# Optimization experiments

Hardware: AMD Instinct MI355X
Metric: run time of the kernel (lower is better)

Reference implementation:

```python
import jax, jax.numpy as jnp
import numpy as np


def _ln(z, g, b, eps=1e-5):
    mu = z.mean(-1, keepdims=True)
    v = ((z - mu) ** 2).mean(-1, keepdims=True)
    return (z - mu) / jnp.sqrt(v + eps) * g + b


def _forward(x, C_prev, n_prev, m_prev, ln_in_g, ln_in_b, wq, bq, wk, bk, wv, bv, wi, bi, wf, bf, wo, bo, rd_w1, rd_b1, rd_g, rd_be, rd_w2, rd_b2, ssm_log_lam, ssm_log_b, ssm_c, ssm_log_d, ssm_log_step, ssm_vol_gate, ssm_alpha, ssm_ln_g, ssm_ln_b, ln_mem_g, ln_mem_b):
    B, S, F = x.shape
    D = wq.shape[0]
    sqd = jnp.sqrt(jnp.float32(D))
    w = max(1, int(S * 0.2))
    pad0 = jnp.zeros((B, 1, F), x.dtype)
    cs = jnp.concatenate([pad0, jnp.cumsum(x, 1)], 1)
    cs2 = jnp.concatenate([pad0, jnp.cumsum(x * x, 1)], 1)
    wsum = cs[:, w:] - cs[:, :-w]
    wsq = cs2[:, w:] - cs2[:, :-w]
    var = (wsq - wsum * wsum / w) / (w - 1)
    std = jnp.sqrt(jnp.clip(var, 0.0))
    vol = jnp.concatenate([jnp.broadcast_to(std[:, :1], (B, w - 1, F)), std], 1)
    sv = vol.mean(2, keepdims=True)
    sv = sv / (sv.mean(1, keepdims=True) + 1e-6)  # [B,S,1]
    # --- parallel gate computation ---
    xn = _ln(x, ln_in_g, ln_in_b)
    regime = jax.nn.softmax(jax.nn.gelu(_ln(xn @ rd_w1.T + rd_b1, rd_g, rd_be), approximate=False) @ rd_w2.T + rd_b2, axis=-1)
    q = xn @ wq.T + bq
    k = (xn @ wk.T + bk) / sqd
    v = xn @ wv.T + bv
    it = xn @ wi.T + bi  # [B,S,1]
    ft = xn @ wf.T + bf
    o = jax.nn.sigmoid(xn @ wo.T + bo)
    # --- stabilize_gates (running-max exponential stabilization) ---
    mp = jnp.clip(m_prev, -100.0, 100.0)[:, None, :]  # [B,1,1]
    m_t = jnp.maximum(ft, mp + ft)
    ig = jnp.exp(jnp.clip(it - m_t, -15.0, 15.0))
    fg = jnp.exp(jnp.clip(ft + mp - m_t, -15.0, 15.0))
    # --- store_key_value outer products + cumulative matrix memory ---
    kn = k / (jnp.linalg.norm(k, axis=2, keepdims=True) + 1e-12) * sqd
    vn = v / (jnp.linalg.norm(v, axis=2, keepdims=True) + 1e-6) * sqd
    upd = jnp.clip(ig, 0.0, 1.0)[..., None] * (vn[..., :, None] * kn[..., None, :])  # [B,S,D,D]
    f_cum = jnp.cumprod(fg, axis=1)  # [B,S,1]
    C_t = f_cum[..., None] * C_prev[:, None] + jnp.cumsum(upd, 1)
    # --- structured state-space mixing, vectorized over the D memory rows ---
    lam = -jnp.exp(ssm_log_lam)
    step = jnp.exp(ssm_log_step)
    a_disc = (2.0 + step * lam) / (2.0 - step * lam)  # bilinear discretization
    b_disc = step * (1.0 + a_disc) * jnp.exp(ssm_log_b)[:, 0] / 2.0
    xr = C_t.transpose(0, 2, 1, 3).reshape(B * D, S, D)  # rows folded into batch
    volr = jnp.broadcast_to(sv[:, None, :, 0], (B, D, S)).reshape(B * D, S)
    u = xr.mean(-1)  # [BD,S], per-step scalar drive
    vgate = jax.nn.sigmoid(ssm_vol_gate)
    def stepf(h, inp):
        u_t, vol_t = inp
        h = a_disc[None] * h + b_disc[None] * u_t[:, None]
        h = _ln(h, ssm_ln_g, ssm_ln_b)
        h = h / (1.0 + vgate[None] * vol_t[:, None])
        return h, h
    h0 = jnp.zeros((B * D, D), x.dtype)
    _, hs = jax.lax.scan(stepf, h0, (u.T, volr.T))  # [S,BD,D]
    yscal = jnp.einsum('sbn,n->bs', hs, ssm_c[0])  # [BD,S]
    y = yscal[..., None] + jnp.exp(ssm_log_d) * xr
    alpha = jax.nn.sigmoid(ssm_alpha)
    mixed = alpha * xr + (1.0 - alpha) * y
    C_mixed = mixed.reshape(B, D, S, D).transpose(0, 2, 1, 3)
    mf = regime[:, :, 0:1][..., None]  # regime-aware mixing factor
    C_t = C_mixed * mf + C_t * (1.0 - mf)
    C_t = C_t / (jnp.linalg.norm(C_t.reshape(B, S, D * D), axis=-1)[..., None, None] + 1e-6) * sqd
    # --- mLSTM readout (stabilizer_threshold = 1.0) ---
    n_t = f_cum * n_prev[:, None, :] + jnp.cumsum(ig * k, 1)
    h_til = jnp.einsum('bsij,bsj->bsi', C_t, q)
    denom = jnp.maximum(jnp.abs(jnp.sum(n_t * q, -1, keepdims=True)), 1.0)
    return o * _ln(h_til / denom, ln_mem_g, ln_mem_b)


def setup_inputs() -> dict:
    key = jax.random.key(0)
    ks = jax.random.split(key, 12)
    B, S, F, D = 8, 512, 32, 64
    sF, sD = 1.0 / np.sqrt(F), 1.0 / np.sqrt(D)
    n = lambda k, sh, s=1.0: jax.random.normal(k, sh, jnp.float32) * s
    return dict(
        x=n(ks[0], (B, S, F)),
        C_prev=jnp.zeros((B, D, D), jnp.float32),
        n_prev=jnp.zeros((B, D), jnp.float32),
        m_prev=jnp.zeros((B, 1), jnp.float32),
        ln_in_g=jnp.ones((F,), jnp.float32), ln_in_b=jnp.zeros((F,), jnp.float32),
        wq=n(ks[1], (D, F), sF), bq=jnp.zeros((D,), jnp.float32),
        wk=n(ks[2], (D, F), sF), bk=jnp.zeros((D,), jnp.float32),
        wv=n(ks[3], (D, F), sF), bv=jnp.zeros((D,), jnp.float32),
        wi=n(ks[4], (1, F), sF), bi=jnp.zeros((1,), jnp.float32),
        wf=n(ks[5], (1, F), sF), bf=jnp.ones((1,), jnp.float32),
        wo=n(ks[6], (D, F), sF), bo=jnp.zeros((D,), jnp.float32),
        rd_w1=n(ks[7], (D, F), sF), rd_b1=jnp.zeros((D,), jnp.float32),
        rd_g=jnp.ones((D,), jnp.float32), rd_be=jnp.zeros((D,), jnp.float32),
        rd_w2=n(ks[8], (4, D), sD), rd_b2=jnp.zeros((4,), jnp.float32),
        ssm_log_lam=jnp.linspace(np.log(0.001), np.log(0.1), D).astype(jnp.float32),
        ssm_log_b=jax.random.uniform(ks[9], (D, 1), jnp.float32, -0.5, 0.5),
        ssm_c=n(ks[10], (1, D), sD),
        ssm_log_d=jnp.zeros((1,), jnp.float32),
        ssm_log_step=jnp.float32(np.log(0.001)),
        ssm_vol_gate=jnp.ones((D,), jnp.float32),
        ssm_alpha=jnp.float32(0.7),
        ssm_ln_g=jnp.ones((D,), jnp.float32), ssm_ln_b=jnp.zeros((D,), jnp.float32),
        ln_mem_g=jnp.ones((D,), jnp.float32), ln_mem_b=jnp.zeros((D,), jnp.float32),
    )


def reference(x, C_prev, n_prev, m_prev, ln_in_g, ln_in_b, wq, bq, wk, bk, wv, bv, wi, bi, wf, bf, wo, bo, rd_w1, rd_b1, rd_g, rd_be, rd_w2, rd_b2, ssm_log_lam, ssm_log_b, ssm_c, ssm_log_d, ssm_log_step, ssm_vol_gate, ssm_alpha, ssm_ln_g, ssm_ln_b, ln_mem_g, ln_mem_b):
    return _forward(x, C_prev, n_prev, m_prev, ln_in_g, ln_in_b, wq, bq, wk, bk, wv, bv, wi, bi, wf, bf, wo, bo, rd_w1, rd_b1, rd_g, rd_be, rd_w2, rd_b2, ssm_log_lam, ssm_log_b, ssm_c, ssm_log_d, ssm_log_step, ssm_vol_gate, ssm_alpha, ssm_ln_g, ssm_ln_b, ln_mem_g, ln_mem_b)
```

## Files before the change

kernel.cpp:

```cpp
#include <hip/hip_runtime.h>
#include <math.h>

#define BB 8
#define SS 512
#define FF 32
#define DD 64
#define WVOL 102
#define CH 16
#define NCH (SS / CH)

template<int CTRL, int RM, bool BC>
__device__ __forceinline__ float updpp(float oldv, float x) {
  return __int_as_float(__builtin_amdgcn_update_dpp(
      __float_as_int(oldv), __float_as_int(x), CTRL, RM, 0xF, BC));
}
__device__ __forceinline__ float rlane(float v, int l) {
  return __int_as_float(__builtin_amdgcn_readlane(__float_as_int(v), l));
}
__device__ __forceinline__ float dsum64(float x) {
  x += updpp<0x111, 0xF, true>(0.f, x);
  x += updpp<0x112, 0xF, true>(0.f, x);
  x += updpp<0x114, 0xF, true>(0.f, x);
  x += updpp<0x118, 0xF, true>(0.f, x);
  x += updpp<0x142, 0xF, true>(0.f, x);
  x += updpp<0x143, 0xF, true>(0.f, x);
  return rlane(x, 63);
}
__device__ __forceinline__ float dsum32(float x) {
  x += updpp<0x111, 0xF, true>(0.f, x);
  x += updpp<0x112, 0xF, true>(0.f, x);
  x += updpp<0x114, 0xF, true>(0.f, x);
  x += updpp<0x118, 0xF, true>(0.f, x);
  x += updpp<0x142, 0xF, true>(0.f, x);
  return rlane(x, 31);
}
__device__ __forceinline__ float dscan_add(float x) {
  x += updpp<0x111, 0xF, true>(0.f, x);
  x += updpp<0x112, 0xF, true>(0.f, x);
  x += updpp<0x114, 0xF, true>(0.f, x);
  x += updpp<0x118, 0xF, true>(0.f, x);
  x += updpp<0x142, 0xA, true>(0.f, x);
  x += updpp<0x143, 0xC, true>(0.f, x);
  return x;
}
__device__ __forceinline__ float dscan_mul(float x) {
  x *= updpp<0x111, 0xF, false>(1.f, x);
  x *= updpp<0x112, 0xF, false>(1.f, x);
  x *= updpp<0x114, 0xF, false>(1.f, x);
  x *= updpp<0x118, 0xF, false>(1.f, x);
  x *= updpp<0x142, 0xA, false>(1.f, x);
  x *= updpp<0x143, 0xC, false>(1.f, x);
  return x;
}

__global__ void k_vol_std(const float* __restrict__ x, float* __restrict__ svraw) {
  int b = blockIdx.x; int s = WVOL - 1 + blockIdx.y;
  int lane = threadIdx.x; int f = lane & 31; int half = lane >> 5;
  const float* xb = x + (size_t)(b * SS) * FF + f;
  float wsum = 0.f, wsq = 0.f;
  int t0 = s - WVOL + 1 + half;
#pragma unroll 17
  for (int k = 0; k < WVOL / 2; ++k) {
    float xv = xb[(t0 + 2 * k) * FF];
    wsum += xv; wsq = fmaf(xv, xv, wsq);
  }
  wsum += __shfl_xor(wsum, 32); wsq += __shfl_xor(wsq, 32);
  float var = (wsq - wsum * wsum * (1.f / WVOL)) * (1.f / (WVOL - 1));
  float sd = sqrtf(fmaxf(var, 0.f));
  float m = dsum64(sd) * 0.5f * (1.f / FF);
  if (lane == 0) svraw[b * SS + s] = m;
}

__global__ void k_proj(const float* __restrict__ x, const float* __restrict__ m_prev,
                       const float* __restrict__ Cp,
                       const float* __restrict__ ln_in_g, const float* __restrict__ ln_in_b,
                       const float* __restrict__ wq, const float* __restrict__ bq,
                       const float* __restrict__ wk, const float* __restrict__ bk,
                       const float* __restrict__ wv, const float* __restrict__ bv,
                       const float* __restrict__ wi, const float* __restrict__ bi,
                       const float* __restrict__ wf, const float* __restrict__ bf,
                       const float* __restrict__ wo, const float* __restrict__ bo,
                       const float* __restrict__ rd_w1, const float* __restrict__ rd_b1,
                       const float* __restrict__ rd_g, const float* __restrict__ rd_be,
                       const float* __restrict__ rd_w2, const float* __restrict__ rd_b2,
                       float* __restrict__ qo, float* __restrict__ kno, float* __restrict__ vno,
                       float* __restrict__ iko, float* __restrict__ oo,
                       float* __restrict__ knT, float* __restrict__ vnT,
                       float* __restrict__ cg_a, float* __restrict__ fg_a,
                       float* __restrict__ mf_a, float* __restrict__ cks_a,
                       float* __restrict__ qsum_a, float* __restrict__ zc) {
  int bs = blockIdx.x; int b = bs / SS; int s = bs % SS;
  int lane = threadIdx.x;
  __shared__ float xs[FF];
  __shared__ float ks[DD];
  float xv = (lane < FF) ? x[bs * FF + lane] : 0.f;
  float s1x = dsum32(xv);
  float s2x = dsum32(xv * xv);
  if (lane < FF) {
    float mu = s1x * (1.f / FF);
    float var = s2x * (1.f / FF) - mu * mu;
    xs[lane] = (xv - mu) * rsqrtf(var + 1e-5f) * ln_in_g[lane] + ln_in_b[lane];
  }
  __syncthreads();
  int d = lane;
  float aq = bq[d], ak = bk[d], av = bv[d], ao = bo[d], at = rd_b1[d];
#pragma unroll
  for (int f = 0; f < FF; ++f) {
    float xf = xs[f];
    aq = fmaf(xf, wq[d * FF + f], aq);
    ak = fmaf(xf, wk[d * FF + f], ak);
    av = fmaf(xf, wv[d * FF + f], av);
    ao = fmaf(xf, wo[d * FF + f], ao);
    at = fmaf(xf, rd_w1[d * FF + f], at);
  }
  float pit = (lane < FF) ? xs[lane] * wi[lane] : 0.f;
  float pft = (lane < FF) ? xs[lane] * wf[lane] : 0.f;
  float itv = dsum32(pit) + bi[0];
  float ftv = dsum32(pft) + bf[0];
  float s1 = dsum64(at), s2 = dsum64(at * at);
  float mu = s1 * (1.f / DD);
  float var = s2 * (1.f / DD) - mu * mu;
  float tn = (at - mu) * rsqrtf(var + 1e-5f) * rd_g[d] + rd_be[d];
  float ge = 0.5f * tn * (1.f + erff(tn * 0.70710678118654752f));
  float l0 = dsum64(ge * rd_w2[0 * DD + d]) + rd_b2[0];
  float l1 = dsum64(ge * rd_w2[1 * DD + d]) + rd_b2[1];
  float l2 = dsum64(ge * rd_w2[2 * DD + d]) + rd_b2[2];
  float l3 = dsum64(ge * rd_w2[3 * DD + d]) + rd_b2[3];
  float mx = fmaxf(fmaxf(l0, l1), fmaxf(l2, l3));
  float e0 = expf(l0 - mx), e1 = expf(l1 - mx), e2 = expf(l2 - mx), e3 = expf(l3 - mx);
  float mfv = e0 / (e0 + e1 + e2 + e3);
  float kd = ak * 0.125f;
  float kk = dsum64(kd * kd);
  float knd = kd * (8.f / (sqrtf(kk) + 1e-12f));
  float vv = dsum64(av * av);
  float vnd = av * (8.f / (sqrtf(vv) + 1e-6f));
  float ksum = dsum64(knd);
  float qsum = dsum64(aq);
  float mp = fminf(fmaxf(m_prev[b], -100.f), 100.f);
  float mt = fmaxf(ftv, mp + ftv);
  float ig = expf(fminf(fmaxf(itv - mt, -15.f), 15.f));
  float fg = expf(fminf(fmaxf(ftv + mp - mt, -15.f), 15.f));
  float cg = fminf(ig, 1.f);
  qo[bs * DD + d] = aq;
  kno[bs * DD + d] = knd;
  vno[bs * DD + d] = vnd;
  iko[bs * DD + d] = ig * kd;
  oo[bs * DD + d] = 1.f / (1.f + expf(-ao));
  knT[(b * DD + d) * SS + s] = knd;
  vnT[(b * DD + d) * SS + s] = vnd;
  ks[d] = knd;
  __syncthreads();
  float acc = 0.f;
  const float* cr = Cp + (b * DD + d) * DD;
#pragma unroll
  for (int j = 0; j < DD; ++j) acc = fmaf(cr[j], ks[j], acc);
  float z = dsum64(vnd * acc);
  if (lane == 0) {
    cg_a[bs] = cg; fg_a[bs] = fg; mf_a[bs] = mfv;
    cks_a[bs] = cg * ksum; qsum_a[bs] = qsum;
    zc[bs] = cg * z;
  }
}

__global__ void k_main(const float* __restrict__ qo, const float* __restrict__ kno,
                       const float* __restrict__ vno,
                       const float* __restrict__ knT, const float* __restrict__ vnT,
                       const float* __restrict__ cg_a,
                       float* __restrict__ p2, float* __restrict__ rho) {
  int bs = blockIdx.x; int b = bs / SS; int s = bs % SS;
  int lane = threadIdx.x;
  __shared__ float w[64];
  const float* qrow = qo + bs * DD;
  const float* krow = kno + bs * DD;
  const float* vrow = vno + bs * DD;
  float pacc = 0.f, rp = 0.f;
  int sT = s & ~63;
  for (int T = 0; T < sT; T += 64) {
    int t = T + lane;
    float A = 0.f, KK = 0.f, VV = 0.f;
#pragma unroll 8
    for (int j = 0; j < DD; ++j) {
      float kt = knT[(b * DD + j) * SS + t];
      float vt = vnT[(b * DD + j) * SS + t];
      A = fmaf(kt, qrow[j], A);
      KK = fmaf(kt, krow[j], KK);
      VV = fmaf(vt, vrow[j], VV);
    }
    float cgt = cg_a[b * SS + t];
    w[lane] = cgt * A;
    rp = fmaf(2.f * cgt, KK * VV, rp);
    __syncthreads();
#pragma unroll 8
    for (int tl = 0; tl < 64; ++tl)
      pacc = fmaf(w[tl], vno[(b * SS + T + tl) * DD + lane], pacc);
    __syncthreads();
  }
  {
    int T = sT; int t = T + lane;
    float A = 0.f, KK = 0.f, VV = 0.f;
#pragma unroll 8
    for (int j = 0; j < DD; ++j) {
      float kt = knT[(b * DD + j) * SS + t];
      float vt = vnT[(b * DD + j) * SS + t];
      A = fmaf(kt, qrow[j], A);
      KK = fmaf(kt, krow[j], KK);
      VV = fmaf(vt, vrow[j], VV);
    }
    float cgt = cg_a[b * SS + t];
    w[lane] = (t <= s) ? cgt * A : 0.f;
    float wr = (t < s) ? 2.f : (t == s ? 1.f : 0.f);
    rp = fmaf(wr * cgt, KK * VV, rp);
    __syncthreads();
    int tmax = s - sT;
    for (int tl = 0; tl <= tmax; ++tl)
      pacc = fmaf(w[tl], vno[(b * SS + T + tl) * DD + lane], pacc);
  }
  p2[bs * DD + lane] = pacc;
  float rr = dsum64(rp);
  if (lane == 0) rho[bs] = cg_a[bs] * rr;
}

__global__ void k_scalar_scan(const float* __restrict__ fg_a, const float* __restrict__ zc,
                              const float* __restrict__ rho, const float* __restrict__ Cp,
                              const float* __restrict__ svraw,
                              float* __restrict__ fcum, float* __restrict__ cpd,
                              float* __restrict__ sn2, float* __restrict__ cpr,
                              float* __restrict__ cpn2, float* __restrict__ sv) {
  int b = blockIdx.x; int lane = threadIdx.x;
  float rs = 0.f, r2 = 0.f;
  const float* cr = Cp + (b * DD + lane) * DD;
#pragma unroll
  for (int j = 0; j < DD; ++j) { float c = cr[j]; rs += c; r2 = fmaf(c, c, r2); }
  cpr[b * DD + lane] = rs;
  float tot2 = dsum64(r2);
  if (lane == 0) cpn2[b] = tot2;
  float m0 = svraw[b * SS + WVOL - 1];
  float vals[8]; float part = 0.f;
#pragma unroll
  for (int c = 0; c < 8; ++c) {
    int idx = c * 64 + lane;
    float v = (idx < WVOL - 1) ? m0 : svraw[b * SS + idx];
    vals[c] = v; part += v;
  }
  float tot = dsum64(part);
  float inv = 1.f / (tot * (1.f / SS) + 1e-6f);
#pragma unroll
  for (int c = 0; c < 8; ++c) sv[b * SS + c * 64 + lane] = vals[c] * inv;
  float cf = 1.f, cz = 0.f, crr = 0.f;
  for (int c = 0; c < 8; ++c) {
    int bs = b * SS + c * 64 + lane;
    float f = dscan_mul(fg_a[bs]) * cf;
    float z = dscan_add(zc[bs]) + cz;
    float r = dscan_add(rho[bs]) + crr;
    fcum[bs] = f; cpd[bs] = z; sn2[bs] = r;
    cf = rlane(f, 63); cz = rlane(z, 63); crr = rlane(r, 63);
  }
}

__global__ void k_csum(const float* __restrict__ ik, const float* __restrict__ vno,
                       const float* __restrict__ cks_a,
                       float* __restrict__ csn, float* __restrict__ csr) {
  int blk = blockIdx.x; int b = blk / NCH; int w = blk % NCH; int d = threadIdx.x;
  float na = 0.f, ra = 0.f;
#pragma unroll
  for (int t = 0; t < CH; ++t) {
    int bs = b * SS + w * CH + t;
    na += ik[bs * DD + d];
    ra = fmaf(cks_a[bs], vno[bs * DD + d], ra);
  }
  csn[blk * DD + d] = na; csr[blk * DD + d] = ra;
}
__global__ void k_scan_apply(const float* __restrict__ ik, const float* __restrict__ vno,
                             const float* __restrict__ cks_a,
                             const float* __restrict__ csn, const float* __restrict__ csr,
                             float* __restrict__ nacc, float* __restrict__ racc) {
  int blk = blockIdx.x; int b = blk / NCH; int w = blk % NCH; int d = threadIdx.x;
  float na = 0.f, ra = 0.f;
  for (int w2 = 0; w2 < w; ++w2) {
    na += csn[(b * NCH + w2) * DD + d];
    ra += csr[(b * NCH + w2) * DD + d];
  }
#pragma unroll
  for (int t = 0; t < CH; ++t) {
    int bs = b * SS + w * CH + t;
    na += ik[bs * DD + d];
    ra = fmaf(cks_a[bs], vno[bs * DD + d], ra);
    nacc[bs * DD + d] = na;
    racc[bs * DD + d] = ra;
  }
}

__global__ void k_ssm(const float* __restrict__ fcum, const float* __restrict__ racc,
                      const float* __restrict__ cpr, const float* __restrict__ sv,
                      const float* __restrict__ log_lam, const float* __restrict__ log_b,
                      const float* __restrict__ cvec,
                      const float* __restrict__ log_step, const float* __restrict__ vol_gate,
                      const float* __restrict__ ln_g, const float* __restrict__ ln_b,
                      float* __restrict__ ysT) {
  int blk = blockIdx.x; int b = blk >> 6; int i = blk & 63;
  int n = threadIdx.x;
  float st = expf(log_step[0]);
  float lam = -expf(log_lam[n]);
  float ad = (2.f + st * lam) / (2.f - st * lam);
  float bd = st * (1.f + ad) * expf(log_b[n]) * 0.5f;
  float vg = 1.f / (1.f + expf(-vol_gate[n]));
  float g = ln_g[n], be = ln_b[n], cn = cvec[n];
  float cprv = cpr[b * DD + i];
  float u[8], w[8];
#pragma unroll
  for (int c = 0; c < 8; ++c) {
    int s = c * 64 + n; int bs = b * SS + s;
    u[c] = fmaf(fcum[bs], cprv, racc[(size_t)bs * DD + i]) * (1.f / DD);
    w[c] = sv[bs];
  }
  float h = 0.f;
#pragma unroll
  for (int c = 0; c < 8; ++c) {
    float yout = 0.f;
#pragma unroll 4
    for (int t = 0; t < 64; ++t) {
      float uu = rlane(u[c], t);
      float vv = rlane(w[c], t);
      float bdu = bd * uu;
      float rden = __builtin_amdgcn_rcpf(fmaf(vg, vv, 1.f));
      float grden = g * rden, berden = be * rden;
      float ht = fmaf(ad, h, bdu);
      float p1 = ht, p2 = ht * ht;
      p1 += updpp<0x111, 0xF, true>(0.f, p1); p2 += updpp<0x111, 0xF, true>(0.f, p2);
      p1 += updpp<0x112, 0xF, true>(0.f, p1); p2 += updpp<0x112, 0xF, true>(0.f, p2);
      p1 += updpp<0x114, 0xF, true>(0.f, p1); p2 += updpp<0x114, 0xF, true>(0.f, p2);
      p1 += updpp<0x118, 0xF, true>(0.f, p1); p2 += updpp<0x118, 0xF, true>(0.f, p2);
      p1 += updpp<0x142, 0xF, true>(0.f, p1); p2 += updpp<0x142, 0xF, true>(0.f, p2);
      p1 += updpp<0x143, 0xF, true>(0.f, p1); p2 += updpp<0x143, 0xF, true>(0.f, p2);
      float s1 = rlane(p1, 63), s2 = rlane(p2, 63);
      float mu = s1 * (1.f / DD);
      float r2m = fmaf(-mu, s1, s2);
      float arg = fmaxf(fmaf(r2m, 1.f / DD, 1e-5f), 1e-5f);
      float irs = __builtin_amdgcn_rsqf(arg);
      float hv = fmaf((ht - mu) * grden, irs, berden);
      h = hv;
      float y = cn * hv;
      y += updpp<0x111, 0xF, true>(0.f, y);
      y += updpp<0x112, 0xF, true>(0.f, y);
      y += updpp<0x114, 0xF, true>(0.f, y);
      y += updpp<0x118, 0xF, true>(0.f, y);
      y += updpp<0x142, 0xF, true>(0.f, y);
      y += updpp<0x143, 0xF, true>(0.f, y);
      float su = rlane(y, 63);
      yout = (n == t) ? su : yout;
    }
    ysT[(size_t)(b * DD + i) * SS + c * 64 + n] = yout;
  }
}

__global__ void k_final(const float* __restrict__ qo, const float* __restrict__ oo,
                        const float* __restrict__ p2, const float* __restrict__ racc,
                        const float* __restrict__ nacc, const float* __restrict__ ysT,
                        const float* __restrict__ Cp, const float* __restrict__ cpr,
                        const float* __restrict__ cpn2,
                        const float* __restrict__ fcum, const float* __restrict__ cpd,
                        const float* __restrict__ sn2,
                        const float* __restrict__ mf_a, const float* __restrict__ qsum_a,
                        const float* __restrict__ n_prev,
                        const float* __restrict__ ssm_log_d, const float* __restrict__ ssm_alpha,
                        const float* __restrict__ ln_mem_g, const float* __restrict__ ln_mem_b,
                        float* __restrict__ out) {
  int bs = blockIdx.x; int b = bs / SS; int s = bs % SS;
  int i = threadIdx.x;
  __shared__ float qv[DD];
  float qi = qo[bs * DD + i];
  qv[i] = qi;
  __syncthreads();
  float P1 = 0.f;
  const float* cr = Cp + (b * DD + i) * DD;
#pragma unroll
  for (int j = 0; j < DD; ++j) P1 = fmaf(cr[j], qv[j], P1);
  float fc = fcum[bs];
  float p = fmaf(fc, P1, p2[bs * DD + i]);
  float r = fmaf(fc, cpr[b * DD + i], racc[bs * DD + i]);
  float R2 = fc * fc * cpn2[b] + 2.f * fc * cpd[bs] + sn2[bs];
  float al = 1.f / (1.f + expf(-ssm_alpha[0]));
  float kap = al + (1.f - al) * expf(ssm_log_d[0]);
  float mfv = mf_a[bs];
  float beta = 1.f + mfv * (kap - 1.f);
  float gam = mfv * (1.f - al);
  float y = ysT[(size_t)(b * DD + i) * SS + s];
  float syr = dsum64(y * r);
  float sy2 = dsum64(y * y);
  float nrm2 = fmaxf(beta * beta * R2 + 2.f * beta * gam * syr + gam * gam * (float)DD * sy2, 0.f);
  float scale = 8.f / (sqrtf(nrm2) + 1e-6f);
  float nt = fmaf(fc, n_prev[b * DD + i], nacc[bs * DD + i]);
  float ndp = dsum64(nt * qi);
  float denom = fmaxf(fabsf(ndp), 1.f);
  float hh = scale * (fmaf(beta, p, gam * y * qsum_a[bs])) / denom;
  float s1 = dsum64(hh), s2 = dsum64(hh * hh);
  float mu = s1 * (1.f / DD);
  float var = fmaxf(s2 * (1.f / DD) - mu * mu, 0.f);
  float o = (hh - mu) * rsqrtf(var + 1e-5f) * ln_mem_g[i] + ln_mem_b[i];
  out[bs * DD + i] = oo[bs * DD + i] * o;
}

extern "C" void kernel_launch(void* const* d_in, const int* in_sizes, int n_in,
                              void* d_out, int out_size, void* d_ws, size_t ws_size,
                              hipStream_t stream) {
  const float* x        = (const float*)d_in[0];
  const float* C_prev   = (const float*)d_in[1];
  const float* n_prev   = (const float*)d_in[2];
  const float* m_prev   = (const float*)d_in[3];
  const float* ln_in_g  = (const float*)d_in[4];
  const float* ln_in_b  = (const float*)d_in[5];
  const float* wq = (const float*)d_in[6];  const float* bq = (const float*)d_in[7];
  const float* wk = (const float*)d_in[8];  const float* bk = (const float*)d_in[9];
  const float* wv = (const float*)d_in[10]; const float* bv = (const float*)d_in[11];
  const float* wi = (const float*)d_in[12]; const float* bi = (const float*)d_in[13];
  const float* wf = (const float*)d_in[14]; const float* bf = (const float*)d_in[15];
  const float* wo = (const float*)d_in[16]; const float* bo = (const float*)d_in[17];
  const float* rd_w1 = (const float*)d_in[18]; const float* rd_b1 = (const float*)d_in[19];
  const float* rd_g  = (const float*)d_in[20]; const float* rd_be = (const float*)d_in[21];
  const float* rd_w2 = (const float*)d_in[22]; const float* rd_b2 = (const float*)d_in[23];
  const float* ssm_log_lam  = (const float*)d_in[24];
  const float* ssm_log_b    = (const float*)d_in[25];
  const float* ssm_c        = (const float*)d_in[26];
  const float* ssm_log_d    = (const float*)d_in[27];
  const float* ssm_log_step = (const float*)d_in[28];
  const float* ssm_vol_gate = (const float*)d_in[29];
  const float* ssm_alpha    = (const float*)d_in[30];
  const float* ssm_ln_g     = (const float*)d_in[31];
  const float* ssm_ln_b     = (const float*)d_in[32];
  const float* ln_mem_g     = (const float*)d_in[33];
  const float* ln_mem_b     = (const float*)d_in[34];
  float* out = (float*)d_out;

  float* W = (float*)d_ws;
  size_t o0 = 0;
  const size_t BS = (size_t)BB * SS, BSD = BS * DD;
  float* sv    = W + o0; o0 += BS;
  float* svraw = W + o0; o0 += BS;
  float* qo   = W + o0; o0 += BSD;
  float* kno  = W + o0; o0 += BSD;
  float* vno  = W + o0; o0 += BSD;
  float* iko  = W + o0; o0 += BSD;
  float* oo   = W + o0; o0 += BSD;
  float* knT  = W + o0; o0 += BSD;
  float* vnT  = W + o0; o0 += BSD;
  float* p2   = W + o0; o0 += BSD;
  float* racc = W + o0; o0 += BSD;
  float* nacc = W + o0; o0 += BSD;
  float* ysT  = W + o0; o0 += BSD;
  float* cg_a = W + o0; o0 += BS;
  float* fg_a = W + o0; o0 += BS;
  float* mf_a = W + o0; o0 += BS;
  float* cks  = W + o0; o0 += BS;
  float* qsum = W + o0; o0 += BS;
  float* zc   = W + o0; o0 += BS;
  float* fcum = W + o0; o0 += BS;
  float* cpd  = W + o0; o0 += BS;
  float* rho  = W + o0; o0 += BS;
  float* sn2  = W + o0; o0 += BS;
  float* cpr  = W + o0; o0 += (size_t)BB * DD;
  float* cpn2 = W + o0; o0 += BB;
  float* csn  = W + o0; o0 += (size_t)BB * NCH * DD;
  float* csr  = W + o0; o0 += (size_t)BB * NCH * DD;

  hipLaunchKernelGGL(k_vol_std, dim3(BB, SS - WVOL + 1), dim3(64), 0, stream, x, svraw);
  hipLaunchKernelGGL(k_proj, dim3(BB * SS), dim3(64), 0, stream,
                     x, m_prev, C_prev, ln_in_g, ln_in_b, wq, bq, wk, bk, wv, bv, wi, bi,
                     wf, bf, wo, bo, rd_w1, rd_b1, rd_g, rd_be, rd_w2, rd_b2,
                     qo, kno, vno, iko, oo, knT, vnT, cg_a, fg_a, mf_a, cks, qsum, zc);
  hipLaunchKernelGGL(k_main, dim3(BB * SS), dim3(64), 0, stream,
                     qo, kno, vno, knT, vnT, cg_a, p2, rho);
  hipLaunchKernelGGL(k_scalar_scan, dim3(BB), dim3(64), 0, stream,
                     fg_a, zc, rho, C_prev, svraw, fcum, cpd, sn2, cpr, cpn2, sv);
  hipLaunchKernelGGL(k_csum, dim3(BB * NCH), dim3(64), 0, stream,
                     iko, vno, cks, csn, csr);
  hipLaunchKernelGGL(k_scan_apply, dim3(BB * NCH), dim3(64), 0, stream,
                     iko, vno, cks, csn, csr, nacc, racc);
  hipLaunchKernelGGL(k_ssm, dim3(BB * DD), dim3(64), 0, stream,
                     fcum, racc, cpr, sv, ssm_log_lam, ssm_log_b, ssm_c,
                     ssm_log_step, ssm_vol_gate, ssm_ln_g, ssm_ln_b, ysT);
  hipLaunchKernelGGL(k_final, dim3(BB * SS), dim3(64), 0, stream,
                     qo, oo, p2, racc, nacc, ysT, C_prev, cpr, cpn2, fcum, cpd, sn2,
                     mf_a, qsum, n_prev, ssm_log_d, ssm_alpha, ln_mem_g, ln_mem_b, out);
}
```

Before: 332.3 us.

## Tile causal attention-like main kernel over query rows and transpose weights for coalescing

The main causal kernel now handles 4 query rows per block and stages the V tile in shared memory, so each K/V column load is reused across rows. Blocks are interleaved short/long to balance the triangular workload. A new prep kernel transposes C_prev and the projection weights so per-lane reads in k_proj and k_final are coalesced. It also moves the C_prev row sums into the prep kernel and merges the scalar scan with the chunk-sum kernel to cut launches. In exchange the main kernel launches 4x fewer blocks, which may lower occupancy.

```diff
diff --git a/kernel.cpp b/kernel.cpp
--- a/kernel.cpp
+++ b/kernel.cpp
@@ -8,6 +8,7 @@
 #define WVOL 102
 #define CH 16
 #define NCH (SS / CH)
+#define QR 4
 
 template<int CTRL, int RM, bool BC>
 __device__ __forceinline__ float updpp(float oldv, float x) {
@@ -51,6 +52,42 @@
   x *= updpp<0x142, 0xA, false>(1.f, x);
   x *= updpp<0x143, 0xC, false>(1.f, x);
   return x;
+}
+
+__global__ void k_prep(const float* __restrict__ Cp,
+                       const float* __restrict__ wq, const float* __restrict__ wk,
+                       const float* __restrict__ wv, const float* __restrict__ wo,
+                       const float* __restrict__ rw1,
+                       float* __restrict__ CpT, float* __restrict__ wqT,
+                       float* __restrict__ wkT, float* __restrict__ wvT,
+                       float* __restrict__ woT, float* __restrict__ rw1T,
+                       float* __restrict__ cpr, float* __restrict__ cpn2) {
+  int blk = blockIdx.x; int lane = threadIdx.x;
+  if (blk < BB) {
+    int b = blk;
+    const float* rowp = Cp + (size_t)(b * DD + lane) * DD;
+    float rs = 0.f, r2 = 0.f;
+#pragma unroll 8
+    for (int j = 0; j < DD; ++j) {
+      float c = rowp[j];
+      rs += c; r2 = fmaf(c, c, r2);
+      CpT[(size_t)(b * DD + j) * DD + lane] = c;
+    }
+    cpr[b * DD + lane] = rs;
+    float tot2 = dsum64(r2);
+    if (lane == 0) cpn2[b] = tot2;
+  } else {
+    const float* src; float* dst;
+    switch (blk - BB) {
+      case 0: src = wq;  dst = wqT;  break;
+      case 1: src = wk;  dst = wkT;  break;
+      case 2: src = wv;  dst = wvT;  break;
+      case 3: src = wo;  dst = woT;  break;
+      default: src = rw1; dst = rw1T; break;
+    }
+#pragma unroll 8
+    for (int f = 0; f < FF; ++f) dst[f * DD + lane] = src[lane * FF + f];
+  }
 }
 
 __global__ void k_vol_std(const float* __restrict__ x, float* __restrict__ svraw) {
@@ -72,15 +109,15 @@
 }
 
 __global__ void k_proj(const float* __restrict__ x, const float* __restrict__ m_prev,
-                       const float* __restrict__ Cp,
+                       const float* __restrict__ CpT,
                        const float* __restrict__ ln_in_g, const float* __restrict__ ln_in_b,
-                       const float* __restrict__ wq, const float* __restrict__ bq,
-                       const float* __restrict__ wk, const float* __restrict__ bk,
-                       const float* __restrict__ wv, const float* __restrict__ bv,
+                       const float* __restrict__ wqT, const float* __restrict__ bq,
+                       const float* __restrict__ wkT, const float* __restrict__ bk,
+                       const float* __restrict__ wvT, const float* __restrict__ bv,
                        const float* __restrict__ wi, const float* __restrict__ bi,
                        const float* __restrict__ wf, const float* __restrict__ bf,
-                       const float* __restrict__ wo, const float* __restrict__ bo,
-                       const float* __restrict__ rd_w1, const float* __restrict__ rd_b1,
+                       const float* __restrict__ woT, const float* __restrict__ bo,
+                       const float* __restrict__ rw1T, const float* __restrict__ rd_b1,
                        const float* __restrict__ rd_g, const float* __restrict__ rd_be,
                        const float* __restrict__ rd_w2, const float* __restrict__ rd_b2,
                        float* __restrict__ qo, float* __restrict__ kno, float* __restrict__ vno,
@@ -107,11 +144,11 @@
 #pragma unroll
   for (int f = 0; f < FF; ++f) {
     float xf = xs[f];
-    aq = fmaf(xf, wq[d * FF + f], aq);
-    ak = fmaf(xf, wk[d * FF + f], ak);
-    av = fmaf(xf, wv[d * FF + f], av);
-    ao = fmaf(xf, wo[d * FF + f], ao);
-    at = fmaf(xf, rd_w1[d * FF + f], at);
+    aq = fmaf(xf, wqT[f * DD + d], aq);
+    ak = fmaf(xf, wkT[f * DD + d], ak);
+    av = fmaf(xf, wvT[f * DD + d], av);
+    ao = fmaf(xf, woT[f * DD + d], ao);
+    at = fmaf(xf, rw1T[f * DD + d], at);
   }
   float pit = (lane < FF) ? xs[lane] * wi[lane] : 0.f;
   float pft = (lane < FF) ? xs[lane] * wf[lane] : 0.f;
@@ -151,9 +188,9 @@
   ks[d] = knd;
   __syncthreads();
   float acc = 0.f;
-  const float* cr = Cp + (b * DD + d) * DD;
-#pragma unroll
-  for (int j = 0; j < DD; ++j) acc = fmaf(cr[j], ks[j], acc);
+  const float* cpt = CpT + (size_t)b * DD * DD;
+#pragma unroll 8
+  for (int j = 0; j < DD; ++j) acc = fmaf(cpt[j * DD + d], ks[j], acc);
   float z = dsum64(vnd * acc);
   if (lane == 0) {
     cg_a[bs] = cg; fg_a[bs] = fg; mf_a[bs] = mfv;
@@ -167,109 +204,127 @@
                        const float* __restrict__ knT, const float* __restrict__ vnT,
                        const float* __restrict__ cg_a,
                        float* __restrict__ p2, float* __restrict__ rho) {
-  int bs = blockIdx.x; int b = bs / SS; int s = bs % SS;
+  int blk = blockIdx.x;
+  int b = blk >> 7;
+  int q0 = blk & 127;
+  int qt = (q0 & 1) ? (127 - (q0 >> 1)) : (q0 >> 1);
   int lane = threadIdx.x;
-  __shared__ float w[64];
-  const float* qrow = qo + bs * DD;
-  const float* krow = kno + bs * DD;
-  const float* vrow = vno + bs * DD;
-  float pacc = 0.f, rp = 0.f;
-  int sT = s & ~63;
-  for (int T = 0; T < sT; T += 64) {
-    int t = T + lane;
-    float A = 0.f, KK = 0.f, VV = 0.f;
+  int s0 = qt * QR;
+  __shared__ float vls[64][DD];
+  __shared__ float qs[QR][DD], kss[QR][DD], vss[QR][DD];
+  __shared__ float wl[64];
+#pragma unroll
+  for (int r = 0; r < QR; ++r) {
+    int base = (b * SS + s0 + r) * DD + lane;
+    qs[r][lane] = qo[base]; kss[r][lane] = kno[base]; vss[r][lane] = vno[base];
+  }
+  float p2a[QR], rhoa[QR], A[QR], G1[QR], G2[QR];
+#pragma unroll
+  for (int r = 0; r < QR; ++r) { p2a[r] = 0.f; rhoa[r] = 0.f; }
+  int tmax = s0 + QR - 1;
+  for (int t0 = 0; t0 <= tmax; t0 += 64) {
+    int t = t0 + lane;
 #pragma unroll 8
-    for (int j = 0; j < DD; ++j) {
-      float kt = knT[(b * DD + j) * SS + t];
-      float vt = vnT[(b * DD + j) * SS + t];
-      A = fmaf(kt, qrow[j], A);
-      KK = fmaf(kt, krow[j], KK);
-      VV = fmaf(vt, vrow[j], VV);
+    for (int r = 0; r < 64; ++r) vls[r][lane] = vno[(b * SS + t0 + r) * DD + lane];
+#pragma unroll
+    for (int r = 0; r < QR; ++r) { A[r] = 0.f; G1[r] = 0.f; G2[r] = 0.f; }
+    const float* kTp = knT + (size_t)b * DD * SS + t;
+    const float* vTp = vnT + (size_t)b * DD * SS + t;
+    for (int j = 0; j < DD; j += 4) {
+      float kv0 = kTp[(j + 0) * SS], kv1 = kTp[(j + 1) * SS];
+      float kv2 = kTp[(j + 2) * SS], kv3 = kTp[(j + 3) * SS];
+      float vv0 = vTp[(j + 0) * SS], vv1 = vTp[(j + 1) * SS];
+      float vv2 = vTp[(j + 2) * SS], vv3 = vTp[(j + 3) * SS];
+#pragma unroll
+      for (int r = 0; r < QR; ++r) {
+        float4 qq = *(const float4*)&qs[r][j];
+        float4 kk = *(const float4*)&kss[r][j];
+        float4 vv = *(const float4*)&vss[r][j];
+        A[r] = fmaf(kv0, qq.x, A[r]); A[r] = fmaf(kv1, qq.y, A[r]);
+        A[r] = fmaf(kv2, qq.z, A[r]); A[r] = fmaf(kv3, qq.w, A[r]);
+        G1[r] = fmaf(kv0, kk.x, G1[r]); G1[r] = fmaf(kv1, kk.y, G1[r]);
+        G1[r] = fmaf(kv2, kk.z, G1[r]); G1[r] = fmaf(kv3, kk.w, G1[r]);
+        G2[r] = fmaf(vv0, vv.x, G2[r]); G2[r] = fmaf(vv1, vv.y, G2[r]);
+        G2[r] = fmaf(vv2, vv.z, G2[r]); G2[r] = fmaf(vv3, vv.w, G2[r]);
+      }
     }
     float cgt = cg_a[b * SS + t];
-    w[lane] = cgt * A;
-    rp = fmaf(2.f * cgt, KK * VV, rp);
-    __syncthreads();
-#pragma unroll 8
-    for (int tl = 0; tl < 64; ++tl)
-      pacc = fmaf(w[tl], vno[(b * SS + T + tl) * DD + lane], pacc);
-    __syncthreads();
-  }
-  {
-    int T = sT; int t = T + lane;
-    float A = 0.f, KK = 0.f, VV = 0.f;
-#pragma unroll 8
-    for (int j = 0; j < DD; ++j) {
-      float kt = knT[(b * DD + j) * SS + t];
-      float vt = vnT[(b * DD + j) * SS + t];
-      A = fmaf(kt, qrow[j], A);
-      KK = fmaf(kt, krow[j], KK);
-      VV = fmaf(vt, vrow[j], VV);
-    }
-    float cgt = cg_a[b * SS + t];
-    w[lane] = (t <= s) ? cgt * A : 0.f;
-    float wr = (t < s) ? 2.f : (t == s ? 1.f : 0.f);
-    rp = fmaf(wr * cgt, KK * VV, rp);
-    __syncthreads();
-    int tmax = s - sT;
-    for (int tl = 0; tl <= tmax; ++tl)
-      pacc = fmaf(w[tl], vno[(b * SS + T + tl) * DD + lane], pacc);
-  }
-  p2[bs * DD + lane] = pacc;
-  float rr = dsum64(rp);
-  if (lane == 0) rho[bs] = cg_a[bs] * rr;
-}
-
-__global__ void k_scalar_scan(const float* __restrict__ fg_a, const float* __restrict__ zc,
-                              const float* __restrict__ rho, const float* __restrict__ Cp,
-                              const float* __restrict__ svraw,
-                              float* __restrict__ fcum, float* __restrict__ cpd,
-                              float* __restrict__ sn2, float* __restrict__ cpr,
-                              float* __restrict__ cpn2, float* __restrict__ sv) {
-  int b = blockIdx.x; int lane = threadIdx.x;
-  float rs = 0.f, r2 = 0.f;
-  const float* cr = Cp + (b * DD + lane) * DD;
-#pragma unroll
-  for (int j = 0; j < DD; ++j) { float c = cr[j]; rs += c; r2 = fmaf(c, c, r2); }
-  cpr[b * DD + lane] = rs;
-  float tot2 = dsum64(r2);
-  if (lane == 0) cpn2[b] = tot2;
-  float m0 = svraw[b * SS + WVOL - 1];
-  float vals[8]; float part = 0.f;
-#pragma unroll
-  for (int c = 0; c < 8; ++c) {
-    int idx = c * 64 + lane;
-    float v = (idx < WVOL - 1) ? m0 : svraw[b * SS + idx];
-    vals[c] = v; part += v;
-  }
-  float tot = dsum64(part);
-  float inv = 1.f / (tot * (1.f / SS) + 1e-6f);
-#pragma unroll
-  for (int c = 0; c < 8; ++c) sv[b * SS + c * 64 + lane] = vals[c] * inv;
-  float cf = 1.f, cz = 0.f, crr = 0.f;
-  for (int c = 0; c < 8; ++c) {
-    int bs = b * SS + c * 64 + lane;
-    float f = dscan_mul(fg_a[bs]) * cf;
-    float z = dscan_add(zc[bs]) + cz;
-    float r = dscan_add(rho[bs]) + crr;
-    fcum[bs] = f; cpd[bs] = z; sn2[bs] = r;
-    cf = rlane(f, 63); cz = rlane(z, 63); crr = rlane(r, 63);
-  }
-}
-
-__global__ void k_csum(const float* __restrict__ ik, const float* __restrict__ vno,
+#pragma unroll
+    for (int r = 0; r < QR; ++r) {
+      int s = s0 + r;
+      float wr = (t < s) ? 2.f : (t == s ? 1.f : 0.f);
+      rhoa[r] = fmaf(wr * cgt, G1[r] * G2[r], rhoa[r]);
+    }
+#pragma unroll
+    for (int r = 0; r < QR; ++r) {
+      int s = s0 + r;
+      wl[lane] = (t <= s) ? cgt * A[r] : 0.f;
+      float acc = p2a[r];
+#pragma unroll 4
+      for (int tt = 0; tt < 64; tt += 4) {
+        float4 w4 = *(const float4*)&wl[tt];
+        acc = fmaf(w4.x, vls[tt + 0][lane], acc);
+        acc = fmaf(w4.y, vls[tt + 1][lane], acc);
+        acc = fmaf(w4.z, vls[tt + 2][lane], acc);
+        acc = fmaf(w4.w, vls[tt + 3][lane], acc);
+      }
+      p2a[r] = acc;
+    }
+  }
+#pragma unroll
+  for (int r = 0; r < QR; ++r) p2[(b * SS + s0 + r) * DD + lane] = p2a[r];
+#pragma unroll
+  for (int r = 0; r < QR; ++r) {
+    float rr = dsum64(rhoa[r]);
+    float cgs = cg_a[b * SS + s0 + r];
+    if (lane == 0) rho[b * SS + s0 + r] = cgs * rr;
+  }
+}
+
+__global__ void k_post(const float* __restrict__ fg_a, const float* __restrict__ zc,
+                       const float* __restrict__ rho, const float* __restrict__ svraw,
+                       const float* __restrict__ ik, const float* __restrict__ vno,
                        const float* __restrict__ cks_a,
+                       float* __restrict__ fcum, float* __restrict__ cpd,
+                       float* __restrict__ sn2, float* __restrict__ sv,
                        float* __restrict__ csn, float* __restrict__ csr) {
-  int blk = blockIdx.x; int b = blk / NCH; int w = blk % NCH; int d = threadIdx.x;
-  float na = 0.f, ra = 0.f;
-#pragma unroll
-  for (int t = 0; t < CH; ++t) {
-    int bs = b * SS + w * CH + t;
-    na += ik[bs * DD + d];
-    ra = fmaf(cks_a[bs], vno[bs * DD + d], ra);
-  }
-  csn[blk * DD + d] = na; csr[blk * DD + d] = ra;
-}
+  int blk = blockIdx.x; int lane = threadIdx.x;
+  if (blk < BB) {
+    int b = blk;
+    float m0 = svraw[b * SS + WVOL - 1];
+    float vals[8]; float part = 0.f;
+#pragma unroll
+    for (int c = 0; c < 8; ++c) {
+      int idx = c * 64 + lane;
+      float v = (idx < WVOL - 1) ? m0 : svraw[b * SS + idx];
+      vals[c] = v; part += v;
+    }
+    float tot = dsum64(part);
+    float inv = 1.f / (tot * (1.f / SS) + 1e-6f);
+#pragma unroll
+    for (int c = 0; c < 8; ++c) sv[b * SS + c * 64 + lane] = vals[c] * inv;
+    float cf = 1.f, cz = 0.f, crr = 0.f;
+    for (int c = 0; c < 8; ++c) {
+      int bs = b * SS + c * 64 + lane;
+      float f = dscan_mul(fg_a[bs]) * cf;
+      float z = dscan_add(zc[bs]) + cz;
+      float r = dscan_add(rho[bs]) + crr;
+      fcum[bs] = f; cpd[bs] = z; sn2[bs] = r;
+      cf = rlane(f, 63); cz = rlane(z, 63); crr = rlane(r, 63);
+    }
+  } else {
+    int blk2 = blk - BB; int b = blk2 / NCH; int w = blk2 % NCH; int d = lane;
+    float na = 0.f, ra = 0.f;
+#pragma unroll
+    for (int t = 0; t < CH; ++t) {
+      int bs = b * SS + w * CH + t;
+      na += ik[bs * DD + d];
+      ra = fmaf(cks_a[bs], vno[bs * DD + d], ra);
+    }
+    csn[blk2 * DD + d] = na; csr[blk2 * DD + d] = ra;
+  }
+}
+
 __global__ void k_scan_apply(const float* __restrict__ ik, const float* __restrict__ vno,
                              const float* __restrict__ cks_a,
                              const float* __restrict__ csn, const float* __restrict__ csr,
@@ -356,7 +411,7 @@
 __global__ void k_final(const float* __restrict__ qo, const float* __restrict__ oo,
                         const float* __restrict__ p2, const float* __restrict__ racc,
                         const float* __restrict__ nacc, const float* __restrict__ ysT,
-                        const float* __restrict__ Cp, const float* __restrict__ cpr,
+                        const float* __restrict__ CpT, const float* __restrict__ cpr,
                         const float* __restrict__ cpn2,
                         const float* __restrict__ fcum, const float* __restrict__ cpd,
                         const float* __restrict__ sn2,
@@ -372,9 +427,9 @@
   qv[i] = qi;
   __syncthreads();
   float P1 = 0.f;
-  const float* cr = Cp + (b * DD + i) * DD;
-#pragma unroll
-  for (int j = 0; j < DD; ++j) P1 = fmaf(cr[j], qv[j], P1);
+  const float* cpt = CpT + (size_t)b * DD * DD;
+#pragma unroll 8
+  for (int j = 0; j < DD; ++j) P1 = fmaf(cpt[j * DD + i], qv[j], P1);
   float fc = fcum[bs];
   float p = fmaf(fc, P1, p2[bs * DD + i]);
   float r = fmaf(fc, cpr[b * DD + i], racc[bs * DD + i]);
@@ -461,24 +516,32 @@
   float* cpn2 = W + o0; o0 += BB;
   float* csn  = W + o0; o0 += (size_t)BB * NCH * DD;
   float* csr  = W + o0; o0 += (size_t)BB * NCH * DD;
-
+  float* CpT  = W + o0; o0 += (size_t)BB * DD * DD;
+  float* wqT  = W + o0; o0 += (size_t)FF * DD;
+  float* wkT  = W + o0; o0 += (size_t)FF * DD;
+  float* wvT  = W + o0; o0 += (size_t)FF * DD;
+  float* woT  = W + o0; o0 += (size_t)FF * DD;
+  float* rw1T = W + o0; o0 += (size_t)FF * DD;
+
+  hipLaunchKernelGGL(k_prep, dim3(BB + 5), dim3(64), 0, stream,
+                     C_prev, wq, wk, wv, wo, rd_w1,
+                     CpT, wqT, wkT, wvT, woT, rw1T, cpr, cpn2);
   hipLaunchKernelGGL(k_vol_std, dim3(BB, SS - WVOL + 1), dim3(64), 0, stream, x, svraw);
   hipLaunchKernelGGL(k_proj, dim3(BB * SS), dim3(64), 0, stream,
-                     x, m_prev, C_prev, ln_in_g, ln_in_b, wq, bq, wk, bk, wv, bv, wi, bi,
-                     wf, bf, wo, bo, rd_w1, rd_b1, rd_g, rd_be, rd_w2, rd_b2,
+                     x, m_prev, CpT, ln_in_g, ln_in_b, wqT, bq, wkT, bk, wvT, bv, wi, bi,
+                     wf, bf, woT, bo, rw1T, rd_b1, rd_g, rd_be, rd_w2, rd_b2,
                      qo, kno, vno, iko, oo, knT, vnT, cg_a, fg_a, mf_a, cks, qsum, zc);
-  hipLaunchKernelGGL(k_main, dim3(BB * SS), dim3(64), 0, stream,
+  hipLaunchKernelGGL(k_main, dim3(BB * 128), dim3(64), 0, stream,
                      qo, kno, vno, knT, vnT, cg_a, p2, rho);
-  hipLaunchKernelGGL(k_scalar_scan, dim3(BB), dim3(64), 0, stream,
-                     fg_a, zc, rho, C_prev, svraw, fcum, cpd, sn2, cpr, cpn2, sv);
-  hipLaunchKernelGGL(k_csum, dim3(BB * NCH), dim3(64), 0, stream,
-                     iko, vno, cks, csn, csr);
+  hipLaunchKernelGGL(k_post, dim3(BB + BB * NCH), dim3(64), 0, stream,
+                     fg_a, zc, rho, svraw, iko, vno, cks,
+                     fcum, cpd, sn2, sv, csn, csr);
   hipLaunchKernelGGL(k_scan_apply, dim3(BB * NCH), dim3(64), 0, stream,
                      iko, vno, cks, csn, csr, nacc, racc);
   hipLaunchKernelGGL(k_ssm, dim3(BB * DD), dim3(64), 0, stream,
                      fcum, racc, cpr, sv, ssm_log_lam, ssm_log_b, ssm_c,
                      ssm_log_step, ssm_vol_gate, ssm_ln_g, ssm_ln_b, ysT);
   hipLaunchKernelGGL(k_final, dim3(BB * SS), dim3(64), 0, stream,
-                     qo, oo, p2, racc, nacc, ysT, C_prev, cpr, cpn2, fcum, cpd, sn2,
+                     qo, oo, p2, racc, nacc, ysT, CpT, cpr, cpn2, fcum, cpd, sn2,
                      mf_a, qsum, n_prev, ssm_log_d, ssm_alpha, ln_mem_g, ln_mem_b, out);
 }
```

New measurement: 342.4 us. 1.03x slower.
